# Kernel tuning notes

Measured on AMD Instinct MI355X. Metric: run time of the kernel, lower is better.

## Reference

```python
import jax, jax.numpy as jnp
import numpy as np

NEG_SLOPE = 0.2
CONV3_NUM, CONV1_NUM, POLY_NUM = 3, 5, 4
FEAT_DIM = CONV3_NUM * 84 + CONV1_NUM * 12 + POLY_NUM * 12  # 360
DN = ('NCHW', 'OIHW', 'NCHW')


def leaky_relu(x):
    return jnp.where(x >= 0, x, NEG_SLOPE * x)


def conv3x3(x, feat):
    # per-sample dynamic 3x3 conv: feat[:, :81] -> kernel [3,3,3,3], feat[:, 81:84] -> bias
    B = x.shape[0]
    k = feat[:, :81].reshape(B, 3, 3, 3, 3)
    b = feat[:, 81:84]

    def one(xi, ki, bi):
        y = jax.lax.conv_general_dilated(xi[None], ki, (1, 1), 'SAME', dimension_numbers=DN)[0]
        return y + bi[:, None, None]

    return leaky_relu(jax.vmap(one)(x, k, b))


def conv1x1(x, feat):
    B = x.shape[0]
    k = feat[:, :9].reshape(B, 3, 3, 1, 1)
    b = feat[:, 9:12]

    def one(xi, ki, bi):
        y = jax.lax.conv_general_dilated(xi[None], ki, (1, 1), 'VALID', dimension_numbers=DN)[0]
        return y + bi[:, None, None]

    return leaky_relu(jax.vmap(one)(x, k, b))


def conv_stack(x, feature):
    residual = x
    for i in range(CONV3_NUM):
        x = conv3x3(x, feature[:, i * 84:(i + 1) * 84])
    off = CONV3_NUM * 84
    for i in range(CONV1_NUM):
        x = conv1x1(x, feature[:, off + i * 12:off + (i + 1) * 12])
    return residual + x


def att_map(feat, h_mat, w_mat, xc):
    # product over POLY_NUM of (a*h + b*w + c*x + d)
    att = jnp.ones_like(xc)
    for i in range(POLY_NUM):
        a = feat[:, i * 4 + 0].reshape(-1, 1, 1, 1)
        b = feat[:, i * 4 + 1].reshape(-1, 1, 1, 1)
        c = feat[:, i * 4 + 2].reshape(-1, 1, 1, 1)
        d = feat[:, i * 4 + 3].reshape(-1, 1, 1, 1)
        att = att * (a * h_mat + b * w_mat + c * xc + d)
    return att


def apply_attention(x, feature):
    H, W = x.shape[2], x.shape[3]
    h_mat = (jnp.arange(H, dtype=x.dtype) / H).reshape(1, 1, H, 1)
    w_mat = (jnp.arange(W, dtype=x.dtype) / W).reshape(1, 1, 1, W)
    off = CONV3_NUM * 84 + CONV1_NUM * 12
    atts = [att_map(feature[:, off + c * POLY_NUM * 4: off + (c + 1) * POLY_NUM * 4],
                    h_mat, w_mat, x[:, c:c + 1]) for c in range(3)]  # R, G, B
    att = jnp.concatenate(atts, axis=1)
    return x * (1 + att)


def setup_inputs() -> dict:
    key = jax.random.key(0)
    k1, k2, k3 = jax.random.split(key, 3)
    x = jax.random.uniform(k1, (8, 3, 512, 512), dtype=jnp.float32)
    thumb_x = jax.random.uniform(k2, (8, 3, 64, 64), dtype=jnp.float32)
    Wm = jax.random.normal(k3, (3, FEAT_DIM), dtype=jnp.float32) * 0.05
    bm = jnp.zeros((FEAT_DIM,), dtype=jnp.float32)
    return {"x": x, "thumb_x": thumb_x, "Wm": Wm, "bm": bm}


def reference(x, thumb_x, Wm, bm):
    # meta: GAP over thumbnail -> linear -> per-sample hypernetwork features [B, 360]
    feature = jnp.mean(thumb_x, axis=(2, 3)) @ Wm + bm
    x = conv_stack(x, feature)
    x = apply_attention(x, feature)
    thumb = conv_stack(thumb_x, feature)
    thumb = apply_attention(thumb, feature)
    return (x, thumb)
```

## Files before the change

kernel.cpp:

```cpp
#include <hip/hip_runtime.h>


#define LEAKY(v) fmaxf((v), 0.2f * (v))

constexpr int STRD = 84;
constexpr int ROWS0 = 22;
constexpr int CHS  = ROWS0 * STRD;
constexpr int BUFSZ = 3 * CHS + 16;

__global__ __launch_bounds__(384) void prep_kernel(
    const float* __restrict__ thumb, const float* __restrict__ Wm,
    const float* __restrict__ bm, float* __restrict__ feat)
{
    const int b = blockIdx.x;
    const int t = threadIdx.x;
    const int ch = t >> 7;
    const int l  = t & 127;
    const float4* p = (const float4*)(thumb + (size_t)b * 3 * 4096);
    float s = 0.f;
#pragma unroll
    for (int k = 0; k < 8; ++k) {
        float4 v = p[ch * 1024 + l + k * 128];
        s += v.x + v.y + v.z + v.w;
    }
    __shared__ float red[384];
    red[t] = s;
    __syncthreads();
    for (int off = 64; off > 0; off >>= 1) {
        if (l < off) red[t] += red[t + off];
        __syncthreads();
    }
    if (t < 360) {
        const float sc = 1.f / 4096.f;
        const float m0 = red[0] * sc, m1 = red[128] * sc, m2 = red[256] * sc;
        feat[b * 360 + t] =
            fmaf(m0, Wm[t], fmaf(m1, Wm[360 + t], fmaf(m2, Wm[720 + t], bm[t])));
    }
}

template<int R>
__device__ __forceinline__ void conv_rows(
    const float* __restrict__ buf, const float* __restrict__ fw,
    int r0, int gx, float4 acc[][3])
{
    const float b0 = fw[81], b1 = fw[82], b2 = fw[83];
#pragma unroll
    for (int j = 0; j < R; ++j) {
        acc[j][0] = make_float4(b0, b0, b0, b0);
        acc[j][1] = make_float4(b1, b1, b1, b1);
        acc[j][2] = make_float4(b2, b2, b2, b2);
    }
    const int gA = (gx < 0) ? 0 : gx;
#pragma unroll
    for (int ich = 0; ich < 3; ++ich) {
#pragma unroll
        for (int ri = 0; ri < R + 2; ++ri) {
            const int idx = ich * CHS + (r0 + 2 + ri) * STRD;
            const float4 A = *(const float4*)&buf[idx + gA];
            const float4 B = *(const float4*)&buf[idx + gx + 4];
            const float4 C = *(const float4*)&buf[idx + gx + 8];
#pragma unroll
            for (int j = 0; j < R; ++j) {
                const int dy = ri - j;
                if (dy < 0 || dy > 2) continue;
#pragma unroll
                for (int oc = 0; oc < 3; ++oc) {
                    const float w0 = fw[oc * 27 + ich * 9 + dy * 3 + 0];
                    const float w1 = fw[oc * 27 + ich * 9 + dy * 3 + 1];
                    const float w2 = fw[oc * 27 + ich * 9 + dy * 3 + 2];
                    float4& a = acc[j][oc];
                    a.x = fmaf(A.w, w0, fmaf(B.x, w1, fmaf(B.y, w2, a.x)));
                    a.y = fmaf(B.x, w0, fmaf(B.y, w1, fmaf(B.z, w2, a.y)));
                    a.z = fmaf(B.y, w0, fmaf(B.z, w1, fmaf(B.w, w2, a.z)));
                    a.w = fmaf(B.z, w0, fmaf(B.w, w1, fmaf(C.x, w2, a.w)));
                }
            }
        }
    }
}

__global__ __launch_bounds__(256, 4) void conv_att_kernel(
    const float* __restrict__ x, const float* __restrict__ thumb,
    const float* __restrict__ feat, float* __restrict__ out)
{
    __shared__ float buf[BUFSZ];

    int id = blockIdx.x;
    const float* src; float* dst; int H, W, b, trow, tcol;
    if (id < 2048) {
        b = id >> 8; const int t = id & 255;
        H = 512; W = 512; trow = (t >> 3) * 16; tcol = (t & 7) * 64;
        src = x; dst = out;
    } else {
        const int i2 = id - 2048;
        b = i2 >> 2; trow = (i2 & 3) * 16; tcol = 0;
        H = 64; W = 64; src = thumb;
        dst = out + (size_t)8 * 3 * 512 * 512;
    }
    const float* fb = feat + b * 360;
    const int tid = threadIdx.x;

    const float* sbg = src + (size_t)b * 3 * H * W;
    for (int q = tid; q < 1056; q += 256) {
        const int c = q / 352;
        const int rem = q - c * 352;
        const int mr = rem >> 4;
        const int k  = rem & 15;
        const int gr = trow + mr - 3;
        const int gc0 = tcol + 4 * k;
        float4 v = make_float4(0.f, 0.f, 0.f, 0.f);
        if ((unsigned)gr < (unsigned)H)
            v = *(const float4*)&sbg[(size_t)c * H * W + (size_t)gr * W + gc0];
        *(float4*)&buf[c * CHS + mr * STRD + 4 * (k + 1)] = v;
    }
    if (tid < 132) {
        const int c = tid / 44;
        const int rem = tid - c * 44;
        const int mr = rem >> 1;
        const int side = rem & 1;
        const int gr = trow + mr - 3;
        const int gc0 = tcol + (side ? 64 : -4);
        const bool rok = (unsigned)gr < (unsigned)H;
        const float* gp = sbg + (size_t)c * H * W + (size_t)(rok ? gr : 0) * W;
        float4 v;
        if (rok && (unsigned)gc0 <= (unsigned)(W - 4)) {
            v = *(const float4*)&gp[gc0];
        } else {
            v.x = (rok && (unsigned)(gc0 + 0) < (unsigned)W) ? gp[gc0 + 0] : 0.f;
            v.y = (rok && (unsigned)(gc0 + 1) < (unsigned)W) ? gp[gc0 + 1] : 0.f;
            v.z = (rok && (unsigned)(gc0 + 2) < (unsigned)W) ? gp[gc0 + 2] : 0.f;
            v.w = (rok && (unsigned)(gc0 + 3) < (unsigned)W) ? gp[gc0 + 3] : 0.f;
        }
        *(float4*)&buf[c * CHS + mr * STRD + (side ? 68 : 0)] = v;
    }
    if (tid < 66) {
        const int c = tid / 22, mr = tid - c * 22;
        *(float4*)&buf[c * CHS + mr * STRD + 72] = make_float4(0.f, 0.f, 0.f, 0.f);
    }
    __syncthreads();

    const int s3 = tid >> 4;
    const int gx3 = 4 * (tid & 15);

    const bool act1 = tid < 180;
    int s1, gx1;
    if (tid < 160) { s1 = tid >> 4; gx1 = 4 * (tid & 15); }
    else { const int v = tid - 160; s1 = v >> 1; gx1 = (v & 1) ? 64 : -4; }
    float4 acc[2][3];
    if (act1) conv_rows<2>(buf, fb, 2 * s1 - 2, gx1, acc);

    float4 res[3];
#pragma unroll
    for (int c = 0; c < 3; ++c)
        res[c] = *(const float4*)&buf[c * CHS + (s3 + 3) * STRD + gx3 + 4];
    __syncthreads();

    if (act1) {
        const int r0 = 2 * s1 - 2;
#pragma unroll
        for (int j = 0; j < 2; ++j)
#pragma unroll
            for (int oc = 0; oc < 3; ++oc) {
                float4 v = acc[j][oc];
                v.x = LEAKY(v.x); v.y = LEAKY(v.y); v.z = LEAKY(v.z); v.w = LEAKY(v.w);
                *(float4*)&buf[oc * CHS + (r0 + j + 3) * STRD + gx1 + 4] = v;
            }
    }
    __syncthreads();

    const bool act2 = tid < 162;
    int s2, gx2;
    if (tid < 144) { s2 = tid >> 4; gx2 = 4 * (tid & 15); }
    else { const int v = tid - 144; s2 = v >> 1; gx2 = (v & 1) ? 64 : -4; }
    if (act2) conv_rows<2>(buf, fb + 84, 2 * s2 - 1, gx2, acc);
    __syncthreads();

    if (act2) {
        const int r0 = 2 * s2 - 1;
#pragma unroll
        for (int j = 0; j < 2; ++j)
#pragma unroll
            for (int oc = 0; oc < 3; ++oc) {
                float4 v = acc[j][oc];
                v.x = LEAKY(v.x); v.y = LEAKY(v.y); v.z = LEAKY(v.z); v.w = LEAKY(v.w);
                *(float4*)&buf[oc * CHS + (r0 + j + 3) * STRD + gx2 + 4] = v;
            }
    }
    __syncthreads();

    float4 y[1][3];
    conv_rows<1>(buf, fb + 168, s3, gx3, y);
    float4 y0 = y[0][0], y1 = y[0][1], y2 = y[0][2];
    y0.x = LEAKY(y0.x); y0.y = LEAKY(y0.y); y0.z = LEAKY(y0.z); y0.w = LEAKY(y0.w);
    y1.x = LEAKY(y1.x); y1.y = LEAKY(y1.y); y1.z = LEAKY(y1.z); y1.w = LEAKY(y1.w);
    y2.x = LEAKY(y2.x); y2.y = LEAKY(y2.y); y2.z = LEAKY(y2.z); y2.w = LEAKY(y2.w);

#pragma unroll
    for (int lay = 0; lay < 5; ++lay) {
        const float* fw = fb + 252 + lay * 12;
        const float w00 = fw[0], w01 = fw[1], w02 = fw[2];
        const float w10 = fw[3], w11 = fw[4], w12 = fw[5];
        const float w20 = fw[6], w21 = fw[7], w22 = fw[8];
        const float c0 = fw[9], c1 = fw[10], c2 = fw[11];
        float4 z0, z1, z2;
        z0.x = fmaf(y0.x, w00, fmaf(y1.x, w01, fmaf(y2.x, w02, c0)));
        z0.y = fmaf(y0.y, w00, fmaf(y1.y, w01, fmaf(y2.y, w02, c0)));
        z0.z = fmaf(y0.z, w00, fmaf(y1.z, w01, fmaf(y2.z, w02, c0)));
        z0.w = fmaf(y0.w, w00, fmaf(y1.w, w01, fmaf(y2.w, w02, c0)));
        z1.x = fmaf(y0.x, w10, fmaf(y1.x, w11, fmaf(y2.x, w12, c1)));
        z1.y = fmaf(y0.y, w10, fmaf(y1.y, w11, fmaf(y2.y, w12, c1)));
        z1.z = fmaf(y0.z, w10, fmaf(y1.z, w11, fmaf(y2.z, w12, c1)));
        z1.w = fmaf(y0.w, w10, fmaf(y1.w, w11, fmaf(y2.w, w12, c1)));
        z2.x = fmaf(y0.x, w20, fmaf(y1.x, w21, fmaf(y2.x, w22, c2)));
        z2.y = fmaf(y0.y, w20, fmaf(y1.y, w21, fmaf(y2.y, w22, c2)));
        z2.z = fmaf(y0.z, w20, fmaf(y1.z, w21, fmaf(y2.z, w22, c2)));
        z2.w = fmaf(y0.w, w20, fmaf(y1.w, w21, fmaf(y2.w, w22, c2)));
        y0.x = LEAKY(z0.x); y0.y = LEAKY(z0.y); y0.z = LEAKY(z0.z); y0.w = LEAKY(z0.w);
        y1.x = LEAKY(z1.x); y1.y = LEAKY(z1.y); y1.z = LEAKY(z1.z); y1.w = LEAKY(z1.w);
        y2.x = LEAKY(z2.x); y2.y = LEAKY(z2.y); y2.z = LEAKY(z2.z); y2.w = LEAKY(z2.w);
    }

    const float invH = 1.f / (float)H;
    const float invW = 1.f / (float)W;
    const int gr = trow + s3;
    const float h = (float)gr * invH;
    const float wbase = (float)(tcol + gx3) * invW;
    const float4 wv = make_float4(wbase, wbase + invW, wbase + 2.f * invW, wbase + 3.f * invW);
#pragma unroll
    for (int ch = 0; ch < 3; ++ch) {
        const float* fp = fb + 312 + ch * 16;
        const float pa0 = fp[0], pb0 = fp[1], pc0 = fp[2], pd0 = fp[3];
        const float pa1 = fp[4], pb1 = fp[5], pc1 = fp[6], pd1 = fp[7];
        const float pa2 = fp[8], pb2 = fp[9], pc2 = fp[10], pd2 = fp[11];
        const float pa3 = fp[12], pb3 = fp[13], pc3 = fp[14], pd3 = fp[15];
        const float4 yv = (ch == 0) ? y0 : (ch == 1) ? y1 : y2;
        float4 v;
        v.x = yv.x + res[ch].x;
        v.y = yv.y + res[ch].y;
        v.z = yv.z + res[ch].z;
        v.w = yv.w + res[ch].w;
        const float t0 = fmaf(pa0, h, pd0), t1 = fmaf(pa1, h, pd1);
        const float t2 = fmaf(pa2, h, pd2), t3 = fmaf(pa3, h, pd3);
        float4 o;
        float a0 = fmaf(pb0, wv.x, fmaf(pc0, v.x, t0));
        a0 *= fmaf(pb1, wv.x, fmaf(pc1, v.x, t1));
        a0 *= fmaf(pb2, wv.x, fmaf(pc2, v.x, t2));
        a0 *= fmaf(pb3, wv.x, fmaf(pc3, v.x, t3));
        o.x = v.x * (1.f + a0);
        float a1 = fmaf(pb0, wv.y, fmaf(pc0, v.y, t0));
        a1 *= fmaf(pb1, wv.y, fmaf(pc1, v.y, t1));
        a1 *= fmaf(pb2, wv.y, fmaf(pc2, v.y, t2));
        a1 *= fmaf(pb3, wv.y, fmaf(pc3, v.y, t3));
        o.y = v.y * (1.f + a1);
        float a2 = fmaf(pb0, wv.z, fmaf(pc0, v.z, t0));
        a2 *= fmaf(pb1, wv.z, fmaf(pc1, v.z, t1));
        a2 *= fmaf(pb2, wv.z, fmaf(pc2, v.z, t2));
        a2 *= fmaf(pb3, wv.z, fmaf(pc3, v.z, t3));
        o.z = v.z * (1.f + a2);
        float a3 = fmaf(pb0, wv.w, fmaf(pc0, v.w, t0));
        a3 *= fmaf(pb1, wv.w, fmaf(pc1, v.w, t1));
        a3 *= fmaf(pb2, wv.w, fmaf(pc2, v.w, t2));
        a3 *= fmaf(pb3, wv.w, fmaf(pc3, v.w, t3));
        o.w = v.w * (1.f + a3);
        *(float4*)&dst[((size_t)(b * 3 + ch) * H + gr) * W + tcol + gx3] = o;
    }
}

extern "C" void kernel_launch(void* const* d_in, const int* in_sizes, int n_in,
                              void* d_out, int out_size, void* d_ws, size_t ws_size,
                              hipStream_t stream) {
    const float* x = (const float*)d_in[0];
    const float* thumb = (const float*)d_in[1];
    const float* Wm = (const float*)d_in[2];
    const float* bm = (const float*)d_in[3];
    float* out = (float*)d_out;
    float* feat = (float*)d_ws;

    prep_kernel<<<8, 384, 0, stream>>>(thumb, Wm, bm, feat);
    conv_att_kernel<<<2080, 256, 0, stream>>>(x, thumb, feat, out);
}
```

Measured before the change: 114.7 us.

## Use packed FP32 FMA over row pairs and halve threads in final stage

Converts the 3x3 conv, 1x1 chain and attention math to 2-wide packed float vectors that pair two adjacent rows, so the compiler can emit packed FMA/mul/max instructions. The final conv3 and pointwise stages now run on 128 threads, each doing two rows, instead of 256 threads doing one row. This aims to cut VALU instruction count roughly in half. In exchange it raises register pressure and leaves half the block idle in the last stage.

```diff
diff --git a/kernel.cpp b/kernel.cpp
--- a/kernel.cpp
+++ b/kernel.cpp
@@ -1,7 +1,12 @@
 #include <hip/hip_runtime.h>
 
 
-#define LEAKY(v) fmaxf((v), 0.2f * (v))
+typedef float v2f __attribute__((ext_vector_type(2)));
+#define FMA2(a, b, c) __builtin_elementwise_fma((a), (b), (c))
+
+__device__ __forceinline__ v2f leaky2(v2f v) {
+    return __builtin_elementwise_max(v, v * 0.2f);
+}
 
 constexpr int STRD = 84;
 constexpr int ROWS0 = 22;
@@ -38,44 +43,68 @@
     }
 }
 
-template<int R>
-__device__ __forceinline__ void conv_rows(
+__device__ __forceinline__ void conv_rows_pk(
     const float* __restrict__ buf, const float* __restrict__ fw,
-    int r0, int gx, float4 acc[][3])
+    int r0, int gx, v2f acc[3][4])
 {
     const float b0 = fw[81], b1 = fw[82], b2 = fw[83];
 #pragma unroll
-    for (int j = 0; j < R; ++j) {
-        acc[j][0] = make_float4(b0, b0, b0, b0);
-        acc[j][1] = make_float4(b1, b1, b1, b1);
-        acc[j][2] = make_float4(b2, b2, b2, b2);
+    for (int c = 0; c < 4; ++c) {
+        v2f i0 = {b0, b0}; v2f i1 = {b1, b1}; v2f i2 = {b2, b2};
+        acc[0][c] = i0; acc[1][c] = i1; acc[2][c] = i2;
     }
     const int gA = (gx < 0) ? 0 : gx;
 #pragma unroll
     for (int ich = 0; ich < 3; ++ich) {
-#pragma unroll
-        for (int ri = 0; ri < R + 2; ++ri) {
+        float4 QA[4], QB[4], QC[4];
+#pragma unroll
+        for (int ri = 0; ri < 4; ++ri) {
             const int idx = ich * CHS + (r0 + 2 + ri) * STRD;
-            const float4 A = *(const float4*)&buf[idx + gA];
-            const float4 B = *(const float4*)&buf[idx + gx + 4];
-            const float4 C = *(const float4*)&buf[idx + gx + 8];
-#pragma unroll
-            for (int j = 0; j < R; ++j) {
-                const int dy = ri - j;
-                if (dy < 0 || dy > 2) continue;
-#pragma unroll
-                for (int oc = 0; oc < 3; ++oc) {
-                    const float w0 = fw[oc * 27 + ich * 9 + dy * 3 + 0];
-                    const float w1 = fw[oc * 27 + ich * 9 + dy * 3 + 1];
-                    const float w2 = fw[oc * 27 + ich * 9 + dy * 3 + 2];
-                    float4& a = acc[j][oc];
-                    a.x = fmaf(A.w, w0, fmaf(B.x, w1, fmaf(B.y, w2, a.x)));
-                    a.y = fmaf(B.x, w0, fmaf(B.y, w1, fmaf(B.z, w2, a.y)));
-                    a.z = fmaf(B.y, w0, fmaf(B.z, w1, fmaf(B.w, w2, a.z)));
-                    a.w = fmaf(B.z, w0, fmaf(B.w, w1, fmaf(C.x, w2, a.w)));
+            QA[ri] = *(const float4*)&buf[idx + gA];
+            QB[ri] = *(const float4*)&buf[idx + gx + 4];
+            QC[ri] = *(const float4*)&buf[idx + gx + 8];
+        }
+#pragma unroll
+        for (int dy = 0; dy < 3; ++dy) {
+            v2f win[6];
+            {
+                v2f a = {QA[dy].w, QA[dy + 1].w}; win[0] = a;
+                v2f b = {QB[dy].x, QB[dy + 1].x}; win[1] = b;
+                v2f c = {QB[dy].y, QB[dy + 1].y}; win[2] = c;
+                v2f d = {QB[dy].z, QB[dy + 1].z}; win[3] = d;
+                v2f e = {QB[dy].w, QB[dy + 1].w}; win[4] = e;
+                v2f f = {QC[dy].x, QC[dy + 1].x}; win[5] = f;
+            }
+#pragma unroll
+            for (int oc = 0; oc < 3; ++oc) {
+                const float w0 = fw[oc * 27 + ich * 9 + dy * 3 + 0];
+                const float w1 = fw[oc * 27 + ich * 9 + dy * 3 + 1];
+                const float w2 = fw[oc * 27 + ich * 9 + dy * 3 + 2];
+                v2f W0 = {w0, w0}; v2f W1 = {w1, w1}; v2f W2 = {w2, w2};
+#pragma unroll
+                for (int c = 0; c < 4; ++c) {
+                    acc[oc][c] = FMA2(win[c], W0,
+                                 FMA2(win[c + 1], W1,
+                                 FMA2(win[c + 2], W2, acc[oc][c])));
                 }
             }
         }
+    }
+}
+
+__device__ __forceinline__ void write_strip_pk(
+    float* __restrict__ buf, int r0, int gx, v2f acc[3][4])
+{
+#pragma unroll
+    for (int oc = 0; oc < 3; ++oc) {
+        v2f l0 = leaky2(acc[oc][0]);
+        v2f l1 = leaky2(acc[oc][1]);
+        v2f l2 = leaky2(acc[oc][2]);
+        v2f l3 = leaky2(acc[oc][3]);
+        float4 ra = make_float4(l0.x, l1.x, l2.x, l3.x);
+        float4 rb = make_float4(l0.y, l1.y, l2.y, l3.y);
+        *(float4*)&buf[oc * CHS + (r0 + 3) * STRD + gx + 4] = ra;
+        *(float4*)&buf[oc * CHS + (r0 + 4) * STRD + gx + 4] = rb;
     }
 }
 
@@ -139,130 +168,110 @@
     }
     __syncthreads();
 
-    const int s3 = tid >> 4;
-    const int gx3 = 4 * (tid & 15);
-
     const bool act1 = tid < 180;
     int s1, gx1;
     if (tid < 160) { s1 = tid >> 4; gx1 = 4 * (tid & 15); }
     else { const int v = tid - 160; s1 = v >> 1; gx1 = (v & 1) ? 64 : -4; }
-    float4 acc[2][3];
-    if (act1) conv_rows<2>(buf, fb, 2 * s1 - 2, gx1, acc);
-
-    float4 res[3];
-#pragma unroll
-    for (int c = 0; c < 3; ++c)
-        res[c] = *(const float4*)&buf[c * CHS + (s3 + 3) * STRD + gx3 + 4];
-    __syncthreads();
-
-    if (act1) {
-        const int r0 = 2 * s1 - 2;
-#pragma unroll
-        for (int j = 0; j < 2; ++j)
-#pragma unroll
-            for (int oc = 0; oc < 3; ++oc) {
-                float4 v = acc[j][oc];
-                v.x = LEAKY(v.x); v.y = LEAKY(v.y); v.z = LEAKY(v.z); v.w = LEAKY(v.w);
-                *(float4*)&buf[oc * CHS + (r0 + j + 3) * STRD + gx1 + 4] = v;
-            }
-    }
+    v2f acc[3][4];
+    if (act1) conv_rows_pk(buf, fb, 2 * s1 - 2, gx1, acc);
+
+    const int s3 = tid >> 4;
+    const int gx3 = 4 * (tid & 15);
+    v2f res2[3][4];
+    if (tid < 128) {
+#pragma unroll
+        for (int ch = 0; ch < 3; ++ch) {
+            float4 ra = *(const float4*)&buf[ch * CHS + (2 * s3 + 3) * STRD + gx3 + 4];
+            float4 rb = *(const float4*)&buf[ch * CHS + (2 * s3 + 4) * STRD + gx3 + 4];
+            v2f p0 = {ra.x, rb.x}; res2[ch][0] = p0;
+            v2f p1 = {ra.y, rb.y}; res2[ch][1] = p1;
+            v2f p2 = {ra.z, rb.z}; res2[ch][2] = p2;
+            v2f p3 = {ra.w, rb.w}; res2[ch][3] = p3;
+        }
+    }
+    __syncthreads();
+
+    if (act1) write_strip_pk(buf, 2 * s1 - 2, gx1, acc);
     __syncthreads();
 
     const bool act2 = tid < 162;
     int s2, gx2;
     if (tid < 144) { s2 = tid >> 4; gx2 = 4 * (tid & 15); }
     else { const int v = tid - 144; s2 = v >> 1; gx2 = (v & 1) ? 64 : -4; }
-    if (act2) conv_rows<2>(buf, fb + 84, 2 * s2 - 1, gx2, acc);
-    __syncthreads();
-
-    if (act2) {
-        const int r0 = 2 * s2 - 1;
-#pragma unroll
-        for (int j = 0; j < 2; ++j)
-#pragma unroll
-            for (int oc = 0; oc < 3; ++oc) {
-                float4 v = acc[j][oc];
-                v.x = LEAKY(v.x); v.y = LEAKY(v.y); v.z = LEAKY(v.z); v.w = LEAKY(v.w);
-                *(float4*)&buf[oc * CHS + (r0 + j + 3) * STRD + gx2 + 4] = v;
-            }
-    }
-    __syncthreads();
-
-    float4 y[1][3];
-    conv_rows<1>(buf, fb + 168, s3, gx3, y);
-    float4 y0 = y[0][0], y1 = y[0][1], y2 = y[0][2];
-    y0.x = LEAKY(y0.x); y0.y = LEAKY(y0.y); y0.z = LEAKY(y0.z); y0.w = LEAKY(y0.w);
-    y1.x = LEAKY(y1.x); y1.y = LEAKY(y1.y); y1.z = LEAKY(y1.z); y1.w = LEAKY(y1.w);
-    y2.x = LEAKY(y2.x); y2.y = LEAKY(y2.y); y2.z = LEAKY(y2.z); y2.w = LEAKY(y2.w);
-
-#pragma unroll
-    for (int lay = 0; lay < 5; ++lay) {
-        const float* fw = fb + 252 + lay * 12;
-        const float w00 = fw[0], w01 = fw[1], w02 = fw[2];
-        const float w10 = fw[3], w11 = fw[4], w12 = fw[5];
-        const float w20 = fw[6], w21 = fw[7], w22 = fw[8];
-        const float c0 = fw[9], c1 = fw[10], c2 = fw[11];
-        float4 z0, z1, z2;
-        z0.x = fmaf(y0.x, w00, fmaf(y1.x, w01, fmaf(y2.x, w02, c0)));
-        z0.y = fmaf(y0.y, w00, fmaf(y1.y, w01, fmaf(y2.y, w02, c0)));
-        z0.z = fmaf(y0.z, w00, fmaf(y1.z, w01, fmaf(y2.z, w02, c0)));
-        z0.w = fmaf(y0.w, w00, fmaf(y1.w, w01, fmaf(y2.w, w02, c0)));
-        z1.x = fmaf(y0.x, w10, fmaf(y1.x, w11, fmaf(y2.x, w12, c1)));
-        z1.y = fmaf(y0.y, w10, fmaf(y1.y, w11, fmaf(y2.y, w12, c1)));
-        z1.z = fmaf(y0.z, w10, fmaf(y1.z, w11, fmaf(y2.z, w12, c1)));
-        z1.w = fmaf(y0.w, w10, fmaf(y1.w, w11, fmaf(y2.w, w12, c1)));
-        z2.x = fmaf(y0.x, w20, fmaf(y1.x, w21, fmaf(y2.x, w22, c2)));
-        z2.y = fmaf(y0.y, w20, fmaf(y1.y, w21, fmaf(y2.y, w22, c2)));
-        z2.z = fmaf(y0.z, w20, fmaf(y1.z, w21, fmaf(y2.z, w22, c2)));
-        z2.w = fmaf(y0.w, w20, fmaf(y1.w, w21, fmaf(y2.w, w22, c2)));
-        y0.x = LEAKY(z0.x); y0.y = LEAKY(z0.y); y0.z = LEAKY(z0.z); y0.w = LEAKY(z0.w);
-        y1.x = LEAKY(z1.x); y1.y = LEAKY(z1.y); y1.z = LEAKY(z1.z); y1.w = LEAKY(z1.w);
-        y2.x = LEAKY(z2.x); y2.y = LEAKY(z2.y); y2.z = LEAKY(z2.z); y2.w = LEAKY(z2.w);
-    }
-
-    const float invH = 1.f / (float)H;
-    const float invW = 1.f / (float)W;
-    const int gr = trow + s3;
-    const float h = (float)gr * invH;
-    const float wbase = (float)(tcol + gx3) * invW;
-    const float4 wv = make_float4(wbase, wbase + invW, wbase + 2.f * invW, wbase + 3.f * invW);
-#pragma unroll
-    for (int ch = 0; ch < 3; ++ch) {
-        const float* fp = fb + 312 + ch * 16;
-        const float pa0 = fp[0], pb0 = fp[1], pc0 = fp[2], pd0 = fp[3];
-        const float pa1 = fp[4], pb1 = fp[5], pc1 = fp[6], pd1 = fp[7];
-        const float pa2 = fp[8], pb2 = fp[9], pc2 = fp[10], pd2 = fp[11];
-        const float pa3 = fp[12], pb3 = fp[13], pc3 = fp[14], pd3 = fp[15];
-        const float4 yv = (ch == 0) ? y0 : (ch == 1) ? y1 : y2;
-        float4 v;
-        v.x = yv.x + res[ch].x;
-        v.y = yv.y + res[ch].y;
-        v.z = yv.z + res[ch].z;
-        v.w = yv.w + res[ch].w;
-        const float t0 = fmaf(pa0, h, pd0), t1 = fmaf(pa1, h, pd1);
-        const float t2 = fmaf(pa2, h, pd2), t3 = fmaf(pa3, h, pd3);
-        float4 o;
-        float a0 = fmaf(pb0, wv.x, fmaf(pc0, v.x, t0));
-        a0 *= fmaf(pb1, wv.x, fmaf(pc1, v.x, t1));
-        a0 *= fmaf(pb2, wv.x, fmaf(pc2, v.x, t2));
-        a0 *= fmaf(pb3, wv.x, fmaf(pc3, v.x, t3));
-        o.x = v.x * (1.f + a0);
-        float a1 = fmaf(pb0, wv.y, fmaf(pc0, v.y, t0));
-        a1 *= fmaf(pb1, wv.y, fmaf(pc1, v.y, t1));
-        a1 *= fmaf(pb2, wv.y, fmaf(pc2, v.y, t2));
-        a1 *= fmaf(pb3, wv.y, fmaf(pc3, v.y, t3));
-        o.y = v.y * (1.f + a1);
-        float a2 = fmaf(pb0, wv.z, fmaf(pc0, v.z, t0));
-        a2 *= fmaf(pb1, wv.z, fmaf(pc1, v.z, t1));
-        a2 *= fmaf(pb2, wv.z, fmaf(pc2, v.z, t2));
-        a2 *= fmaf(pb3, wv.z, fmaf(pc3, v.z, t3));
-        o.z = v.z * (1.f + a2);
-        float a3 = fmaf(pb0, wv.w, fmaf(pc0, v.w, t0));
-        a3 *= fmaf(pb1, wv.w, fmaf(pc1, v.w, t1));
-        a3 *= fmaf(pb2, wv.w, fmaf(pc2, v.w, t2));
-        a3 *= fmaf(pb3, wv.w, fmaf(pc3, v.w, t3));
-        o.w = v.w * (1.f + a3);
-        *(float4*)&dst[((size_t)(b * 3 + ch) * H + gr) * W + tcol + gx3] = o;
+    if (act2) conv_rows_pk(buf, fb + 84, 2 * s2 - 1, gx2, acc);
+    __syncthreads();
+
+    if (act2) write_strip_pk(buf, 2 * s2 - 1, gx2, acc);
+    __syncthreads();
+
+    if (tid < 128) {
+        v2f y[3][4];
+        {
+            v2f acc3[3][4];
+            conv_rows_pk(buf, fb + 168, 2 * s3, gx3, acc3);
+#pragma unroll
+            for (int oc = 0; oc < 3; ++oc)
+#pragma unroll
+                for (int c = 0; c < 4; ++c) y[oc][c] = leaky2(acc3[oc][c]);
+        }
+
+#pragma unroll
+        for (int lay = 0; lay < 5; ++lay) {
+            const float* fw = fb + 252 + lay * 12;
+            v2f W0 = {fw[0], fw[0]}; v2f W1 = {fw[1], fw[1]}; v2f W2 = {fw[2], fw[2]};
+            v2f W3 = {fw[3], fw[3]}; v2f W4 = {fw[4], fw[4]}; v2f W5 = {fw[5], fw[5]};
+            v2f W6 = {fw[6], fw[6]}; v2f W7 = {fw[7], fw[7]}; v2f W8 = {fw[8], fw[8]};
+            v2f C0 = {fw[9], fw[9]}; v2f C1 = {fw[10], fw[10]}; v2f C2 = {fw[11], fw[11]};
+            v2f z0[4], z1[4], z2[4];
+#pragma unroll
+            for (int c = 0; c < 4; ++c) {
+                z0[c] = FMA2(y[0][c], W0, FMA2(y[1][c], W1, FMA2(y[2][c], W2, C0)));
+                z1[c] = FMA2(y[0][c], W3, FMA2(y[1][c], W4, FMA2(y[2][c], W5, C1)));
+                z2[c] = FMA2(y[0][c], W6, FMA2(y[1][c], W7, FMA2(y[2][c], W8, C2)));
+            }
+#pragma unroll
+            for (int c = 0; c < 4; ++c) {
+                y[0][c] = leaky2(z0[c]);
+                y[1][c] = leaky2(z1[c]);
+                y[2][c] = leaky2(z2[c]);
+            }
+        }
+
+        const float invH = 1.f / (float)H;
+        const float invW = 1.f / (float)W;
+        const int gr0 = trow + 2 * s3;
+        v2f h2 = {(float)gr0 * invH, (float)(gr0 + 1) * invH};
+        const float wb = (float)(tcol + gx3) * invW;
+        const v2f one = {1.f, 1.f};
+#pragma unroll
+        for (int ch = 0; ch < 3; ++ch) {
+            const float* fp = fb + 312 + ch * 16;
+            v2f PA0 = {fp[0], fp[0]},  PB0 = {fp[1], fp[1]},  PC0 = {fp[2], fp[2]},  PD0 = {fp[3], fp[3]};
+            v2f PA1 = {fp[4], fp[4]},  PB1 = {fp[5], fp[5]},  PC1 = {fp[6], fp[6]},  PD1 = {fp[7], fp[7]};
+            v2f PA2 = {fp[8], fp[8]},  PB2 = {fp[9], fp[9]},  PC2 = {fp[10], fp[10]}, PD2 = {fp[11], fp[11]};
+            v2f PA3 = {fp[12], fp[12]}, PB3 = {fp[13], fp[13]}, PC3 = {fp[14], fp[14]}, PD3 = {fp[15], fp[15]};
+            v2f t0 = FMA2(PA0, h2, PD0);
+            v2f t1 = FMA2(PA1, h2, PD1);
+            v2f t2 = FMA2(PA2, h2, PD2);
+            v2f t3 = FMA2(PA3, h2, PD3);
+            v2f o[4];
+#pragma unroll
+            for (int c = 0; c < 4; ++c) {
+                const float wcs = wb + (float)c * invW;
+                v2f Wc = {wcs, wcs};
+                v2f v = y[ch][c] + res2[ch][c];
+                v2f a = FMA2(PB0, Wc, FMA2(PC0, v, t0));
+                a = a * FMA2(PB1, Wc, FMA2(PC1, v, t1));
+                a = a * FMA2(PB2, Wc, FMA2(PC2, v, t2));
+                a = a * FMA2(PB3, Wc, FMA2(PC3, v, t3));
+                o[c] = v * (one + a);
+            }
+            float4 ra = make_float4(o[0].x, o[1].x, o[2].x, o[3].x);
+            float4 rb = make_float4(o[0].y, o[1].y, o[2].y, o[3].y);
+            float* dp = &dst[((size_t)(b * 3 + ch) * H + gr0) * W + tcol + gx3];
+            *(float4*)dp = ra;
+            *(float4*)(dp + W) = rb;
+        }
     }
 }
 
```

New measurement: 111.8 us. 2.5% less time.
